# Kernel tuning notes

Measured on AMD Instinct MI355X. Metric: run time of the kernel, lower is better.

## Reference

```python
import jax, jax.numpy as jnp
import numpy as np

IGNORE_INDEX = -100
VOCAB = 32000
D_MODEL = 2048


def setup_inputs() -> dict:
    key = jax.random.key(0)
    k1, k2, k3 = jax.random.split(key, 3)
    outputs = jax.random.normal(k1, (4, 2048, D_MODEL), dtype=jnp.float32)
    targets = jax.random.randint(k2, (4, 2048), 0, VOCAB, dtype=jnp.int64)
    # LM-head projection weight (torch nn.Linear stores [out_features, in_features]; no bias for LM heads)
    weight = jax.random.normal(k3, (VOCAB, D_MODEL), dtype=jnp.float32) * (D_MODEL ** -0.5)
    return {"outputs": outputs, "targets": targets, "weight": weight}


def reference(outputs, targets, weight):
    # Flatten tokens: [B, S, D] -> [N, D], [B, S] -> [N]
    d = outputs.shape[-1]
    hidden = outputs.reshape(-1, d)
    tgt = targets.reshape(-1)
    valid = tgt != IGNORE_INDEX
    safe_tgt = jnp.where(valid, tgt, 0)

    # Linear projection fused conceptually with CE; per-chunk sum-reduction CE
    # summed over chunks equals the full-batch sum, so we compute it vectorized.
    logits = jnp.einsum("nd,vd->nv", hidden, weight).astype(jnp.float32)  # [N, V]
    logp = jax.nn.log_softmax(logits, axis=-1)
    nll = -jnp.take_along_axis(logp, safe_tgt[:, None], axis=-1)[:, 0]  # [N]

    total_valid = jnp.sum(valid)
    total_loss = jnp.sum(jnp.where(valid, nll, 0.0))
    # forward returns 0.0 when no valid tokens; guard the division
    return jnp.where(total_valid > 0, total_loss / jnp.maximum(total_valid, 1).astype(total_loss.dtype), 0.0)
```

## Files before the change

kernel.cpp:

```cpp
#include <hip/hip_runtime.h>
#include <hip/hip_bf16.h>
#include <math.h>

#define D_MODEL 2048
#define VOCAB   32000
#define NTOK    8192
#define BM      128
#define BN      128
#define BKB     128
#define BK      32
#define LDK     (BK + 8)
#define MTILES  (NTOK / BM)
#define NTILES  (VOCAB / BN)
#define NCHUNK  (VOCAB / 64)

typedef __attribute__((ext_vector_type(8))) short  frag8;
typedef __attribute__((ext_vector_type(4))) float  f32x4;
typedef __attribute__((ext_vector_type(4))) int    i32x4;
typedef __attribute__((ext_vector_type(8))) int    i32x8;


__device__ inline void g2l16(const void* g, void* l) {
    __builtin_amdgcn_global_load_lds(
        (const __attribute__((address_space(1))) unsigned int*)g,
        (__attribute__((address_space(3))) unsigned int*)l,
        16, 0, 0);
}

__device__ inline unsigned pack_bf16(float x, float y) {
    union { float f; unsigned u; } a, b;
    a.f = x; b.f = y;
    return __builtin_amdgcn_perm(b.u, a.u, 0x07060302u);
}


__global__ void cvt_fp8_kernel(const float* __restrict__ src, unsigned char* __restrict__ dst) {
    size_t i = (size_t)blockIdx.x * 256 + threadIdx.x;
    float4 v0 = ((const float4*)src)[2 * i];
    float4 v1 = ((const float4*)src)[2 * i + 1];
    int lo = 0, hi = 0;
    lo = __builtin_amdgcn_cvt_pk_fp8_f32(v0.x, v0.y, lo, 0);
    lo = __builtin_amdgcn_cvt_pk_fp8_f32(v0.z, v0.w, lo, 1);
    hi = __builtin_amdgcn_cvt_pk_fp8_f32(v1.x, v1.y, hi, 0);
    hi = __builtin_amdgcn_cvt_pk_fp8_f32(v1.z, v1.w, hi, 1);
    uint2 o = { (unsigned)lo, (unsigned)hi };
    ((uint2*)dst)[i] = o;
}


__global__ __launch_bounds__(256, 3)
void gemm_lse_fp8(const unsigned char* __restrict__ Hq, const unsigned char* __restrict__ Wq,
                  float* __restrict__ partials) {
    __shared__ unsigned char As[BM * BKB];
    __shared__ unsigned char Bs[BN * BKB];

    const int bid   = blockIdx.x;
    const int mtile = bid & (MTILES - 1);
    const int ntile = bid >> 6;
    const int m0 = mtile * BM;
    const int n0 = ntile * BN;

    const int tid  = threadIdx.x;
    const int lane = tid & 63;
    const int w    = tid >> 6;
    const int wm   = (w >> 1) * 64;
    const int wn   = (w & 1)  * 64;
    const int q    = lane >> 4;
    const int c    = lane & 15;

    const int srow = w * 32 + (lane >> 3);
    const int soff = ((lane & 7) ^ (srow & 7)) * 16;
    const unsigned char* gA = Hq + (size_t)(m0 + srow) * D_MODEL + soff;
    const unsigned char* gB = Wq + (size_t)(n0 + srow) * D_MODEL + soff;
    unsigned char* lA = As + (w * 32) * BKB;
    unsigned char* lB = Bs + (w * 32) * BKB;

    const int plo = (2 * q) ^ (c & 7);

    f32x4 acc[4][4];
    const f32x4 zero = {0.f, 0.f, 0.f, 0.f};
    #pragma unroll
    for (int i = 0; i < 4; ++i)
        #pragma unroll
        for (int j = 0; j < 4; ++j) acc[i][j] = zero;

    #pragma unroll 1
    for (int kt = 0; kt < D_MODEL / BKB; ++kt) {
        const size_t k0 = (size_t)kt * BKB;
        #pragma unroll
        for (int t = 0; t < 4; ++t)
            g2l16(gA + k0 + (size_t)(t * 8) * D_MODEL, lA + t * 8 * BKB);
        #pragma unroll
        for (int t = 0; t < 4; ++t)
            g2l16(gB + k0 + (size_t)(t * 8) * D_MODEL, lB + t * 8 * BKB);
        __syncthreads();

        union Frag { i32x8 v; i32x4 h[2]; };
        i32x8 a8[4], b8[4];
        #pragma unroll
        for (int t = 0; t < 4; ++t) {
            const unsigned char* pa = As + (wm + t * 16 + c) * BKB;
            Frag f;
            f.h[0] = *(const i32x4*)(pa + plo * 16);
            f.h[1] = *(const i32x4*)(pa + (plo ^ 1) * 16);
            a8[t] = f.v;
        }
        #pragma unroll
        for (int t = 0; t < 4; ++t) {
            const unsigned char* pb = Bs + (wn + t * 16 + c) * BKB;
            Frag f;
            f.h[0] = *(const i32x4*)(pb + plo * 16);
            f.h[1] = *(const i32x4*)(pb + (plo ^ 1) * 16);
            b8[t] = f.v;
        }

        #pragma unroll
        for (int tm = 0; tm < 4; ++tm)
            #pragma unroll
            for (int tn = 0; tn < 4; ++tn)
                acc[tm][tn] = __builtin_amdgcn_mfma_scale_f32_16x16x128_f8f6f4(
                    a8[tm], b8[tn], acc[tm][tn],
                    0, 0,
                    0, 0x7F7F7F7F,
                    0, 0x7F7F7F7F);
        __syncthreads();
    }

    const int chunk = ntile * 2 + (w & 1);
    #pragma unroll
    for (int tm = 0; tm < 4; ++tm) {
        #pragma unroll
        for (int r = 0; r < 4; ++r) {
            float v0 = acc[tm][0][r], v1 = acc[tm][1][r];
            float v2 = acc[tm][2][r], v3 = acc[tm][3][r];
            float mx = fmaxf(fmaxf(v0, v1), fmaxf(v2, v3));
            #pragma unroll
            for (int mask = 1; mask <= 8; mask <<= 1)
                mx = fmaxf(mx, __shfl_xor(mx, mask, 64));
            float sm = __expf(v0 - mx) + __expf(v1 - mx)
                     + __expf(v2 - mx) + __expf(v3 - mx);
            #pragma unroll
            for (int mask = 1; mask <= 8; mask <<= 1)
                sm += __shfl_xor(sm, mask, 64);
            if (c == 0) {
                int row_g = m0 + wm + tm * 16 + q * 4 + r;
                float* p = partials + ((size_t)row_g * NCHUNK + chunk) * 2;
                p[0] = mx;
                p[1] = sm;
            }
        }
    }
}


__global__ __launch_bounds__(256, 2)
void gemm_lse_f32(const float* __restrict__ H, const float* __restrict__ W,
                  float* __restrict__ partials) {
    __shared__ unsigned short As[BM][LDK];
    __shared__ unsigned short Bs[BN][LDK];

    const int GM = 8;
    int bid   = blockIdx.x;
    int super = bid / (GM * NTILES);
    int rem   = bid % (GM * NTILES);
    int mtile = super * GM + (rem % GM);
    int ntile = rem / GM;

    const int m0 = mtile * BM;
    const int n0 = ntile * BN;

    const int tid  = threadIdx.x;
    const int lane = tid & 63;
    const int w    = tid >> 6;
    const int wm   = (w >> 1) * 64;
    const int wn   = (w & 1)  * 64;
    const int q    = lane >> 4;
    const int c    = lane & 15;

    f32x4 acc[4][4];
    const f32x4 zero = {0.f, 0.f, 0.f, 0.f};
    #pragma unroll
    for (int i = 0; i < 4; ++i)
        #pragma unroll
        for (int j = 0; j < 4; ++j) acc[i][j] = zero;

    for (int kt = 0; kt < D_MODEL / BK; ++kt) {
        const int k0 = kt * BK;
        #pragma unroll
        for (int s = 0; s < 4; ++s) {
            int i   = tid + s * 256;
            int row = i >> 3;
            int kq  = (i & 7) << 2;

            const float4* pa = (const float4*)(H + (size_t)(m0 + row) * D_MODEL + k0 + kq);
            float4 va = *pa;
            uint2 ba = { pack_bf16(va.x, va.y), pack_bf16(va.z, va.w) };
            *(uint2*)&As[row][kq] = ba;

            const float4* pb = (const float4*)(W + (size_t)(n0 + row) * D_MODEL + k0 + kq);
            float4 vb = *pb;
            uint2 bb = { pack_bf16(vb.x, vb.y), pack_bf16(vb.z, vb.w) };
            *(uint2*)&Bs[row][kq] = bb;
        }
        __syncthreads();

        frag8 af[4], bf[4];
        #pragma unroll
        for (int t = 0; t < 4; ++t)
            af[t] = *(const frag8*)&As[wm + t * 16 + c][q * 8];
        #pragma unroll
        for (int t = 0; t < 4; ++t)
            bf[t] = *(const frag8*)&Bs[wn + t * 16 + c][q * 8];

        #pragma unroll
        for (int tm = 0; tm < 4; ++tm)
            #pragma unroll
            for (int tn = 0; tn < 4; ++tn)
                acc[tm][tn] = __builtin_amdgcn_mfma_f32_16x16x32_bf16(
                    af[tm], bf[tn], acc[tm][tn], 0, 0, 0);
        __syncthreads();
    }

    const int chunk = ntile * 2 + (w & 1);
    #pragma unroll
    for (int tm = 0; tm < 4; ++tm) {
        #pragma unroll
        for (int r = 0; r < 4; ++r) {
            float v0 = acc[tm][0][r], v1 = acc[tm][1][r];
            float v2 = acc[tm][2][r], v3 = acc[tm][3][r];
            float mx = fmaxf(fmaxf(v0, v1), fmaxf(v2, v3));
            #pragma unroll
            for (int mask = 1; mask <= 8; mask <<= 1)
                mx = fmaxf(mx, __shfl_xor(mx, mask, 64));
            float sm = __expf(v0 - mx) + __expf(v1 - mx)
                     + __expf(v2 - mx) + __expf(v3 - mx);
            #pragma unroll
            for (int mask = 1; mask <= 8; mask <<= 1)
                sm += __shfl_xor(sm, mask, 64);
            if (c == 0) {
                int row_g = m0 + wm + tm * 16 + q * 4 + r;
                float* p = partials + ((size_t)row_g * NCHUNK + chunk) * 2;
                p[0] = mx;
                p[1] = sm;
            }
        }
    }
}


__global__ __launch_bounds__(256)
void tgt_kernel(const float* __restrict__ H, const float* __restrict__ W,
                const int* __restrict__ targets, float* __restrict__ tgt_logit) {
    int token = blockIdx.x * 4 + (threadIdx.x >> 6);
    int lane  = threadIdx.x & 63;

    int t  = targets[token];
    int tt = (t == -100) ? 0 : t;
    const float4* h  = (const float4*)(H + (size_t)token * D_MODEL);
    const float4* wr = (const float4*)(W + (size_t)tt * D_MODEL);
    float p = 0.f;
    #pragma unroll
    for (int j = lane; j < D_MODEL / 4; j += 64) {
        float4 a = h[j], b = wr[j];
        p += a.x * b.x + a.y * b.y + a.z * b.z + a.w * b.w;
    }
    #pragma unroll
    for (int mask = 1; mask < 64; mask <<= 1)
        p += __shfl_xor(p, mask, 64);
    if (lane == 0) tgt_logit[token] = p;
}

__device__ inline void lse_merge(float& m, float& s, float om, float os) {
    if (om > m) { s = s * __expf(m - om) + os; m = om; }
    else        { s += os * __expf(om - m); }
}

__global__ __launch_bounds__(256)
void reduce_kernel(const float* __restrict__ partials,
                   const float* __restrict__ tgt_logit,
                   const int* __restrict__ targets,
                   float* __restrict__ nll) {
    int token = blockIdx.x * 4 + (threadIdx.x >> 6);
    int lane  = threadIdx.x & 63;

    float m = -INFINITY, s = 0.f;
    const float* base = partials + (size_t)token * NCHUNK * 2;
    for (int ch = lane; ch < NCHUNK; ch += 64) {
        float2 p = ((const float2*)base)[ch];
        lse_merge(m, s, p.x, p.y);
    }
    #pragma unroll
    for (int mask = 1; mask < 64; mask <<= 1) {
        float om = __shfl_xor(m, mask, 64);
        float os = __shfl_xor(s, mask, 64);
        lse_merge(m, s, om, os);
    }
    if (lane == 0) {
        int t = targets[token];
        nll[token] = (t != -100) ? (m + __logf(s) - tgt_logit[token]) : 0.0f;
    }
}

__global__ __launch_bounds__(256)
void final_kernel(const float* __restrict__ nll, const int* __restrict__ targets,
                  float* __restrict__ out) {
    int tid = threadIdx.x;
    float sum = 0.f, cnt = 0.f;
    for (int i = tid; i < NTOK; i += 256) {
        sum += nll[i];
        cnt += (targets[i] != -100) ? 1.0f : 0.0f;
    }
    #pragma unroll
    for (int mask = 1; mask < 64; mask <<= 1) {
        sum += __shfl_xor(sum, mask, 64);
        cnt += __shfl_xor(cnt, mask, 64);
    }
    __shared__ float lsum[4], lcnt[4];
    int lane = tid & 63, wid = tid >> 6;
    if (lane == 0) { lsum[wid] = sum; lcnt[wid] = cnt; }
    __syncthreads();
    if (tid == 0) {
        float S = lsum[0] + lsum[1] + lsum[2] + lsum[3];
        float C = lcnt[0] + lcnt[1] + lcnt[2] + lcnt[3];
        out[0] = (C > 0.f) ? (S / C) : 0.f;
    }
}


extern "C" void kernel_launch(void* const* d_in, const int* in_sizes, int n_in,
                              void* d_out, int out_size, void* d_ws, size_t ws_size,
                              hipStream_t stream) {
    (void)in_sizes; (void)n_in; (void)out_size;
    const float* H       = (const float*)d_in[0];
    const int*   targets = (const int*)d_in[1];
    const float* W       = (const float*)d_in[2];
    float*       out     = (float*)d_out;

    char* ws = (char*)d_ws;
    const size_t H8_BYTES   = (size_t)NTOK  * D_MODEL;
    const size_t W8_BYTES   = (size_t)VOCAB * D_MODEL;
    const size_t PART_BYTES = (size_t)NTOK * NCHUNK * 2 * 4;
    const size_t NEED = H8_BYTES + W8_BYTES + PART_BYTES + (size_t)NTOK * 8 + 64;

    if (ws_size >= NEED) {
        unsigned char* Hq = (unsigned char*)ws;
        unsigned char* Wq = (unsigned char*)(ws + H8_BYTES);
        float* partials   = (float*)(ws + H8_BYTES + W8_BYTES);
        float* tgt_logit  = (float*)(ws + H8_BYTES + W8_BYTES + PART_BYTES);
        float* nll        = tgt_logit + NTOK;

        cvt_fp8_kernel<<<(NTOK  * D_MODEL / 8) / 256, 256, 0, stream>>>(H, Hq);
        cvt_fp8_kernel<<<(VOCAB * D_MODEL / 8) / 256, 256, 0, stream>>>(W, Wq);
        gemm_lse_fp8<<<MTILES * NTILES, 256, 0, stream>>>(Hq, Wq, partials);
        tgt_kernel<<<NTOK / 4, 256, 0, stream>>>(H, W, targets, tgt_logit);
        reduce_kernel<<<NTOK / 4, 256, 0, stream>>>(partials, tgt_logit, targets, nll);
        final_kernel<<<1, 256, 0, stream>>>(nll, targets, out);
    } else {
        float* partials  = (float*)ws;
        float* tgt_logit = (float*)(ws + PART_BYTES);
        float* nll       = tgt_logit + NTOK;

        gemm_lse_f32<<<MTILES * NTILES, 256, 0, stream>>>(H, W, partials);
        tgt_kernel<<<NTOK / 4, 256, 0, stream>>>(H, W, targets, tgt_logit);
        reduce_kernel<<<NTOK / 4, 256, 0, stream>>>(partials, tgt_logit, targets, nll);
        final_kernel<<<1, 256, 0, stream>>>(nll, targets, out);
    }
}
```

Before: 984.6 us.

## Rewrite FP8 GEMM-LSE with 256x256 tiles and 4-stage async LDS pipeline

Replaces the FP8 GEMM+logsumexp kernel with a 512-thread version that uses 256x256 output tiles, a 4-deep ring of 64-wide K sub-stages loaded with global_load_lds, and explicit vmcnt waits so loads for later stages overlap MFMA work. It also remaps block indices into 8 interleaved groups, presumably for XCD/L2 locality, and raises MFMA wave priority. The larger tiles cut global and LDS traffic per FLOP. In exchange it needs 128 KB of dynamic LDS and many more accumulator registers, which limits occupancy, and correctness depends on the hand-written swizzle and wait counts.

```diff
diff --git a/kernel.cpp b/kernel.cpp
--- a/kernel.cpp
+++ b/kernel.cpp
@@ -5,14 +5,22 @@
 #define D_MODEL 2048
 #define VOCAB   32000
 #define NTOK    8192
+#define NCHUNK  (VOCAB / 64)
+
 #define BM      128
 #define BN      128
-#define BKB     128
 #define BK      32
 #define LDK     (BK + 8)
 #define MTILES  (NTOK / BM)
 #define NTILES  (VOCAB / BN)
-#define NCHUNK  (VOCAB / 64)
+
+#define BM2     256
+#define BN2     256
+#define SUBK    64
+#define NSUB    (D_MODEL / SUBK)
+#define SUBSZ   32768
+#define MT2     (NTOK / BM2)
+#define NT2     (VOCAB / BN2)
 
 typedef __attribute__((ext_vector_type(8))) short  frag8;
 typedef __attribute__((ext_vector_type(4))) float  f32x4;
@@ -48,15 +56,150 @@
 }
 
 
-__global__ __launch_bounds__(256, 3)
-void gemm_lse_fp8(const unsigned char* __restrict__ Hq, const unsigned char* __restrict__ Wq,
+__global__ __launch_bounds__(512, 2)
+void gemm_lse_fp8_v2(const unsigned char* __restrict__ Hq, const unsigned char* __restrict__ Wq,
+                     float* __restrict__ partials) {
+    extern __shared__ unsigned char lds[];
+
+    const int L     = (blockIdx.x & 7) * 500 + (blockIdx.x >> 3);
+    const int mtile = L & 31;
+    const int ntile = L >> 5;
+    const int m0 = mtile * BM2;
+    const int n0 = ntile * BN2;
+
+    const int tid  = threadIdx.x;
+    const int lane = tid & 63;
+    const int w    = tid >> 6;
+    const int wr   = w >> 2;
+    const int wc   = w & 3;
+    const int q    = lane >> 4;
+    const int c    = lane & 15;
+
+    const int sline = tid >> 3;
+    const int sp    = (tid & 7) ^ (sline & 7);
+    const int srow  = 2 * sline + (sp >> 2);
+    const int sjj   = sp & 3;
+    const unsigned char* gA = Hq + (size_t)(m0 + srow) * D_MODEL + sjj * 16;
+    const unsigned char* gB = Wq + (size_t)(n0 + srow) * D_MODEL + sjj * 16;
+    const unsigned wbase = (unsigned)w * 1024;
+
+    const int prow = c >> 1;
+    const int qh   = q >> 1;
+    const int qb   = q & 1;
+    const unsigned sA    = (unsigned)((((c & 1) << 2) | (qb << 1)) ^ prow) << 4;
+    const unsigned aoff0 = (unsigned)(wr * 64 + prow) * 128 + sA;
+    const unsigned aoff1 = aoff0 ^ 16;
+    const unsigned boff0 = 16384u + (unsigned)(wc * 32 + prow) * 128 + sA;
+    const unsigned boff1 = boff0 ^ 16;
+
+    f32x4 acc[8][4];
+    const f32x4 zero = {0.f, 0.f, 0.f, 0.f};
+    #pragma unroll
+    for (int i = 0; i < 8; ++i)
+        #pragma unroll
+        for (int j = 0; j < 4; ++j) acc[i][j] = zero;
+
+    auto STAGE = [&](int s) {
+        const unsigned base = (unsigned)(s & 3) * (unsigned)SUBSZ;
+        const size_t ko = (size_t)s * SUBK;
+        g2l16(gA + ko,                           lds + base + wbase);
+        g2l16(gA + ko + (size_t)128 * D_MODEL,   lds + base + 8192 + wbase);
+        g2l16(gB + ko,                           lds + base + 16384 + wbase);
+        g2l16(gB + ko + (size_t)128 * D_MODEL,   lds + base + 24576 + wbase);
+    };
+
+    STAGE(0); STAGE(1); STAGE(2); STAGE(3);
+
+    union Frag { i32x8 v; i32x4 h[2]; };
+
+    #pragma unroll 1
+    for (int t = 0; t < 16; ++t) {
+        if (t == 15) asm volatile("s_waitcnt vmcnt(0)" ::: "memory");
+        else         asm volatile("s_waitcnt vmcnt(8)" ::: "memory");
+        __builtin_amdgcn_s_barrier();
+
+        const unsigned ring   = (unsigned)(t & 1) * (2u * SUBSZ);
+        const unsigned subsel = ring + (unsigned)qh * SUBSZ;
+        const unsigned char* a0 = lds + subsel + aoff0;
+        const unsigned char* a1 = lds + subsel + aoff1;
+        const unsigned char* b0 = lds + subsel + boff0;
+        const unsigned char* b1 = lds + subsel + boff1;
+
+        i32x8 a8[8], b8[4];
+        #pragma unroll
+        for (int ni = 0; ni < 4; ++ni) {
+            Frag f;
+            f.h[0] = *(const i32x4*)(b0 + ni * 1024);
+            f.h[1] = *(const i32x4*)(b1 + ni * 1024);
+            b8[ni] = f.v;
+        }
+        #pragma unroll
+        for (int mi = 0; mi < 8; ++mi) {
+            Frag f;
+            f.h[0] = *(const i32x4*)(a0 + mi * 1024);
+            f.h[1] = *(const i32x4*)(a1 + mi * 1024);
+            a8[mi] = f.v;
+        }
+
+        asm volatile("s_waitcnt lgkmcnt(0)" ::: "memory");
+        __builtin_amdgcn_sched_barrier(0);
+        __builtin_amdgcn_s_barrier();
+
+        if (t < 14) { STAGE(2 * t + 4); STAGE(2 * t + 5); }
+
+        __builtin_amdgcn_s_setprio(1);
+        #pragma unroll
+        for (int mi = 0; mi < 8; ++mi)
+            #pragma unroll
+            for (int ni = 0; ni < 4; ++ni)
+                acc[mi][ni] = __builtin_amdgcn_mfma_scale_f32_16x16x128_f8f6f4(
+                    a8[mi], b8[ni], acc[mi][ni],
+                    0, 0,
+                    0, 0x7F7F7F7F,
+                    0, 0x7F7F7F7F);
+        __builtin_amdgcn_s_setprio(0);
+    }
+
+    const int chunk = ntile * 4 + wc;
+    #pragma unroll
+    for (int mi = 0; mi < 8; ++mi) {
+        #pragma unroll
+        for (int r = 0; r < 4; ++r) {
+            float v0 = acc[mi][0][r], v1 = acc[mi][1][r];
+            float v2 = acc[mi][2][r], v3 = acc[mi][3][r];
+            float mx = fmaxf(fmaxf(v0, v1), fmaxf(v2, v3));
+            #pragma unroll
+            for (int mask = 1; mask <= 8; mask <<= 1)
+                mx = fmaxf(mx, __shfl_xor(mx, mask, 64));
+            float sm = __expf(v0 - mx) + __expf(v1 - mx)
+                     + __expf(v2 - mx) + __expf(v3 - mx);
+            #pragma unroll
+            for (int mask = 1; mask <= 8; mask <<= 1)
+                sm += __shfl_xor(sm, mask, 64);
+            if (c == 0) {
+                int row_g = m0 + wr * 128 + mi * 16 + q * 4 + r;
+                float* p = partials + ((size_t)row_g * NCHUNK + chunk) * 2;
+                p[0] = mx;
+                p[1] = sm;
+            }
+        }
+    }
+}
+
+
+__global__ __launch_bounds__(256, 2)
+void gemm_lse_f32(const float* __restrict__ H, const float* __restrict__ W,
                   float* __restrict__ partials) {
-    __shared__ unsigned char As[BM * BKB];
-    __shared__ unsigned char Bs[BN * BKB];
-
-    const int bid   = blockIdx.x;
-    const int mtile = bid & (MTILES - 1);
-    const int ntile = bid >> 6;
+    __shared__ unsigned short As[BM][LDK];
+    __shared__ unsigned short Bs[BN][LDK];
+
+    const int GM = 8;
+    int bid   = blockIdx.x;
+    int super = bid / (GM * NTILES);
+    int rem   = bid % (GM * NTILES);
+    int mtile = super * GM + (rem % GM);
+    int ntile = rem / GM;
+
     const int m0 = mtile * BM;
     const int n0 = ntile * BN;
 
@@ -68,15 +211,6 @@
     const int q    = lane >> 4;
     const int c    = lane & 15;
 
-    const int srow = w * 32 + (lane >> 3);
-    const int soff = ((lane & 7) ^ (srow & 7)) * 16;
-    const unsigned char* gA = Hq + (size_t)(m0 + srow) * D_MODEL + soff;
-    const unsigned char* gB = Wq + (size_t)(n0 + srow) * D_MODEL + soff;
-    unsigned char* lA = As + (w * 32) * BKB;
-    unsigned char* lB = Bs + (w * 32) * BKB;
-
-    const int plo = (2 * q) ^ (c & 7);
-
     f32x4 acc[4][4];
     const f32x4 zero = {0.f, 0.f, 0.f, 0.f};
     #pragma unroll
@@ -84,45 +218,40 @@
         #pragma unroll
         for (int j = 0; j < 4; ++j) acc[i][j] = zero;
 
-    #pragma unroll 1
-    for (int kt = 0; kt < D_MODEL / BKB; ++kt) {
-        const size_t k0 = (size_t)kt * BKB;
+    for (int kt = 0; kt < D_MODEL / BK; ++kt) {
+        const int k0 = kt * BK;
+        #pragma unroll
+        for (int s = 0; s < 4; ++s) {
+            int i   = tid + s * 256;
+            int row = i >> 3;
+            int kq  = (i & 7) << 2;
+
+            const float4* pa = (const float4*)(H + (size_t)(m0 + row) * D_MODEL + k0 + kq);
+            float4 va = *pa;
+            uint2 ba = { pack_bf16(va.x, va.y), pack_bf16(va.z, va.w) };
+            *(uint2*)&As[row][kq] = ba;
+
+            const float4* pb = (const float4*)(W + (size_t)(n0 + row) * D_MODEL + k0 + kq);
+            float4 vb = *pb;
+            uint2 bb = { pack_bf16(vb.x, vb.y), pack_bf16(vb.z, vb.w) };
+            *(uint2*)&Bs[row][kq] = bb;
+        }
+        __syncthreads();
+
+        frag8 af[4], bf[4];
         #pragma unroll
         for (int t = 0; t < 4; ++t)
-            g2l16(gA + k0 + (size_t)(t * 8) * D_MODEL, lA + t * 8 * BKB);
+            af[t] = *(const frag8*)&As[wm + t * 16 + c][q * 8];
         #pragma unroll
         for (int t = 0; t < 4; ++t)
-            g2l16(gB + k0 + (size_t)(t * 8) * D_MODEL, lB + t * 8 * BKB);
-        __syncthreads();
-
-        union Frag { i32x8 v; i32x4 h[2]; };
-        i32x8 a8[4], b8[4];
-        #pragma unroll
-        for (int t = 0; t < 4; ++t) {
-            const unsigned char* pa = As + (wm + t * 16 + c) * BKB;
-            Frag f;
-            f.h[0] = *(const i32x4*)(pa + plo * 16);
-            f.h[1] = *(const i32x4*)(pa + (plo ^ 1) * 16);
-            a8[t] = f.v;
-        }
-        #pragma unroll
-        for (int t = 0; t < 4; ++t) {
-            const unsigned char* pb = Bs + (wn + t * 16 + c) * BKB;
-            Frag f;
-            f.h[0] = *(const i32x4*)(pb + plo * 16);
-            f.h[1] = *(const i32x4*)(pb + (plo ^ 1) * 16);
-            b8[t] = f.v;
-        }
+            bf[t] = *(const frag8*)&Bs[wn + t * 16 + c][q * 8];
 
         #pragma unroll
         for (int tm = 0; tm < 4; ++tm)
             #pragma unroll
             for (int tn = 0; tn < 4; ++tn)
-                acc[tm][tn] = __builtin_amdgcn_mfma_scale_f32_16x16x128_f8f6f4(
-                    a8[tm], b8[tn], acc[tm][tn],
-                    0, 0,
-                    0, 0x7F7F7F7F,
-                    0, 0x7F7F7F7F);
+                acc[tm][tn] = __builtin_amdgcn_mfma_f32_16x16x32_bf16(
+                    af[tm], bf[tn], acc[tm][tn], 0, 0, 0);
         __syncthreads();
     }
 
@@ -153,101 +282,6 @@
 }
 
 
-__global__ __launch_bounds__(256, 2)
-void gemm_lse_f32(const float* __restrict__ H, const float* __restrict__ W,
-                  float* __restrict__ partials) {
-    __shared__ unsigned short As[BM][LDK];
-    __shared__ unsigned short Bs[BN][LDK];
-
-    const int GM = 8;
-    int bid   = blockIdx.x;
-    int super = bid / (GM * NTILES);
-    int rem   = bid % (GM * NTILES);
-    int mtile = super * GM + (rem % GM);
-    int ntile = rem / GM;
-
-    const int m0 = mtile * BM;
-    const int n0 = ntile * BN;
-
-    const int tid  = threadIdx.x;
-    const int lane = tid & 63;
-    const int w    = tid >> 6;
-    const int wm   = (w >> 1) * 64;
-    const int wn   = (w & 1)  * 64;
-    const int q    = lane >> 4;
-    const int c    = lane & 15;
-
-    f32x4 acc[4][4];
-    const f32x4 zero = {0.f, 0.f, 0.f, 0.f};
-    #pragma unroll
-    for (int i = 0; i < 4; ++i)
-        #pragma unroll
-        for (int j = 0; j < 4; ++j) acc[i][j] = zero;
-
-    for (int kt = 0; kt < D_MODEL / BK; ++kt) {
-        const int k0 = kt * BK;
-        #pragma unroll
-        for (int s = 0; s < 4; ++s) {
-            int i   = tid + s * 256;
-            int row = i >> 3;
-            int kq  = (i & 7) << 2;
-
-            const float4* pa = (const float4*)(H + (size_t)(m0 + row) * D_MODEL + k0 + kq);
-            float4 va = *pa;
-            uint2 ba = { pack_bf16(va.x, va.y), pack_bf16(va.z, va.w) };
-            *(uint2*)&As[row][kq] = ba;
-
-            const float4* pb = (const float4*)(W + (size_t)(n0 + row) * D_MODEL + k0 + kq);
-            float4 vb = *pb;
-            uint2 bb = { pack_bf16(vb.x, vb.y), pack_bf16(vb.z, vb.w) };
-            *(uint2*)&Bs[row][kq] = bb;
-        }
-        __syncthreads();
-
-        frag8 af[4], bf[4];
-        #pragma unroll
-        for (int t = 0; t < 4; ++t)
-            af[t] = *(const frag8*)&As[wm + t * 16 + c][q * 8];
-        #pragma unroll
-        for (int t = 0; t < 4; ++t)
-            bf[t] = *(const frag8*)&Bs[wn + t * 16 + c][q * 8];
-
-        #pragma unroll
-        for (int tm = 0; tm < 4; ++tm)
-            #pragma unroll
-            for (int tn = 0; tn < 4; ++tn)
-                acc[tm][tn] = __builtin_amdgcn_mfma_f32_16x16x32_bf16(
-                    af[tm], bf[tn], acc[tm][tn], 0, 0, 0);
-        __syncthreads();
-    }
-
-    const int chunk = ntile * 2 + (w & 1);
-    #pragma unroll
-    for (int tm = 0; tm < 4; ++tm) {
-        #pragma unroll
-        for (int r = 0; r < 4; ++r) {
-            float v0 = acc[tm][0][r], v1 = acc[tm][1][r];
-            float v2 = acc[tm][2][r], v3 = acc[tm][3][r];
-            float mx = fmaxf(fmaxf(v0, v1), fmaxf(v2, v3));
-            #pragma unroll
-            for (int mask = 1; mask <= 8; mask <<= 1)
-                mx = fmaxf(mx, __shfl_xor(mx, mask, 64));
-            float sm = __expf(v0 - mx) + __expf(v1 - mx)
-                     + __expf(v2 - mx) + __expf(v3 - mx);
-            #pragma unroll
-            for (int mask = 1; mask <= 8; mask <<= 1)
-                sm += __shfl_xor(sm, mask, 64);
-            if (c == 0) {
-                int row_g = m0 + wm + tm * 16 + q * 4 + r;
-                float* p = partials + ((size_t)row_g * NCHUNK + chunk) * 2;
-                p[0] = mx;
-                p[1] = sm;
-            }
-        }
-    }
-}
-
-
 __global__ __launch_bounds__(256)
 void tgt_kernel(const float* __restrict__ H, const float* __restrict__ W,
                 const int* __restrict__ targets, float* __restrict__ tgt_logit) {
@@ -349,9 +383,16 @@
         float* tgt_logit  = (float*)(ws + H8_BYTES + W8_BYTES + PART_BYTES);
         float* nll        = tgt_logit + NTOK;
 
+        static bool attr_done = false;
+        if (!attr_done) {
+            (void)hipFuncSetAttribute(reinterpret_cast<const void*>(gemm_lse_fp8_v2),
+                                      hipFuncAttributeMaxDynamicSharedMemorySize, 131072);
+            attr_done = true;
+        }
+
         cvt_fp8_kernel<<<(NTOK  * D_MODEL / 8) / 256, 256, 0, stream>>>(H, Hq);
         cvt_fp8_kernel<<<(VOCAB * D_MODEL / 8) / 256, 256, 0, stream>>>(W, Wq);
-        gemm_lse_fp8<<<MTILES * NTILES, 256, 0, stream>>>(Hq, Wq, partials);
+        gemm_lse_fp8_v2<<<MT2 * NT2, 512, 131072, stream>>>(Hq, Wq, partials);
         tgt_kernel<<<NTOK / 4, 256, 0, stream>>>(H, W, targets, tgt_logit);
         reduce_kernel<<<NTOK / 4, 256, 0, stream>>>(partials, tgt_logit, targets, nll);
         final_kernel<<<1, 256, 0, stream>>>(nll, targets, out);
```

New measurement: 1.263 ms. 1.28x slower.
